# Kernel optimization log

Hardware: AMD Instinct MI355X
Metric: run time of the kernel (lower is better)

The kernel has to match this reference:

```python
import jax, jax.numpy as jnp
import numpy as np

N = 50000
E = 800000
DIM = 256
HEADS = 4
HDIM = DIM // HEADS  # 64
NEG_SLOPE = 0.2
LN_EPS = 1e-5


def _layernorm(x, g, b):
    mu = jnp.mean(x, axis=-1, keepdims=True)
    var = jnp.var(x, axis=-1, keepdims=True)
    return (x - mu) * jax.lax.rsqrt(var + LN_EPS) * g + b


def setup_inputs() -> dict:
    key = jax.random.key(0)
    ks = jax.random.split(key, 10)
    x = jax.random.normal(ks[0], (N, DIM), dtype=jnp.float32)
    edge_index = jax.random.randint(ks[1], (2, E), 0, N, dtype=jnp.int64)
    s = 0.05
    W = jax.random.normal(ks[2], (DIM, DIM), dtype=jnp.float32) * s       # GAT linear (heads*out = dim)
    a_src = jax.random.normal(ks[3], (HEADS, HDIM), dtype=jnp.float32) * s
    a_dst = jax.random.normal(ks[4], (HEADS, HDIM), dtype=jnp.float32) * s
    gat_b = jnp.zeros((DIM,), dtype=jnp.float32)
    ln_g = jnp.ones((DIM,), dtype=jnp.float32)
    ln_b = jnp.zeros((DIM,), dtype=jnp.float32)
    W1 = jax.random.normal(ks[5], (DIM, 4 * DIM), dtype=jnp.float32) * s
    b1 = jnp.zeros((4 * DIM,), dtype=jnp.float32)
    W2 = jax.random.normal(ks[6], (4 * DIM, DIM), dtype=jnp.float32) * s
    b2 = jnp.zeros((DIM,), dtype=jnp.float32)
    return {"x": x, "edge_index": edge_index, "W": W, "a_src": a_src,
            "a_dst": a_dst, "gat_b": gat_b, "ln_g": ln_g, "ln_b": ln_b,
            "W1": W1, "b1": b1, "W2": W2, "b2": b2}


def _gat(x, edge_index, W, a_src, a_dst, gat_b):
    # project and split heads: [N, H, C]
    h = (x @ W).reshape(N, HEADS, HDIM)
    alpha_src = jnp.einsum('nhc,hc->nh', h, a_src)  # [N, H]
    alpha_dst = jnp.einsum('nhc,hc->nh', h, a_dst)  # [N, H]
    src = edge_index[0]
    dst = edge_index[1]
    e = jax.nn.leaky_relu(alpha_src[src] + alpha_dst[dst], NEG_SLOPE)  # [E, H]
    # segment softmax over edges sharing a destination node
    m = jax.ops.segment_max(e, dst, num_segments=N)                   # [N, H]
    ex = jnp.exp(e - m[dst])
    denom = jax.ops.segment_sum(ex, dst, num_segments=N)              # [N, H]
    alpha = ex / (denom[dst] + 1e-16)                                 # [E, H]
    msg = h[src] * alpha[:, :, None]                                  # [E, H, C]
    out = jax.ops.segment_sum(msg.reshape(E, DIM), dst, num_segments=N)
    return out + gat_b


def reference(x, edge_index, W, a_src, a_dst, gat_b, ln_g, ln_b, W1, b1, W2, b2):
    residual = x
    g = _gat(x, edge_index, W, a_src, a_dst, gat_b)
    x = _layernorm(x + g, ln_g, ln_b)
    ffn = jax.nn.gelu(x @ W1 + b1, approximate=False) @ W2 + b2
    x = _layernorm(x + ffn, ln_g, ln_b)  # same norm params reused, as in source
    return x + residual
```

## Files before the change

### kernel.cpp

```cpp
#include <hip/hip_runtime.h>
#include <hip/hip_bf16.h>
#include <math.h>

typedef __bf16 bf16;
typedef bf16 bf16x8 __attribute__((ext_vector_type(8)));
typedef float floatx4 __attribute__((ext_vector_type(4)));

#define NN 50000
#define EE 800000
#define DIMC 256
#define FFC 1024

typedef __attribute__((address_space(3))) unsigned int lds_u32;
typedef __attribute__((address_space(1))) unsigned int gbl_u32;

static __device__ __forceinline__ void glds16(const bf16* g, bf16* l) {
    __builtin_amdgcn_global_load_lds((const gbl_u32*)g, (lds_u32*)l, 16, 0, 0);
}

static __device__ __forceinline__ unsigned short f2b(float f) {
    bf16 b = (bf16)f;
    return __builtin_bit_cast(unsigned short, b);
}
static __device__ __forceinline__ float b2f_lo(unsigned u) { return __uint_as_float(u << 16); }
static __device__ __forceinline__ float b2f_hi(unsigned u) { return __uint_as_float(u & 0xffff0000u); }

static __device__ __forceinline__ float gelu_f(float v) {
    float z = -1.5957691216f * v - 0.0713548163f * v * v * v;
    return v / (1.f + __expf(z));
}

__global__ __launch_bounds__(256)
void k_cast_bf16(const float* __restrict__ in, bf16* __restrict__ out, long n4) {
    long i = (long)blockIdx.x * 256 + threadIdx.x;
    if (i >= n4) return;
    float4 v = ((const float4*)in)[i];
    uint2 p;
    p.x = (unsigned)f2b(v.x) | ((unsigned)f2b(v.y) << 16);
    p.y = (unsigned)f2b(v.z) | ((unsigned)f2b(v.w) << 16);
    ((uint2*)out)[i] = p;
}

__global__ __launch_bounds__(256)
void k_tcast(const float* __restrict__ in, bf16* __restrict__ out, int K, int Nc) {
    __shared__ float t[32][33];
    int n0 = blockIdx.x * 32, k0 = blockIdx.y * 32;
    int tx = threadIdx.x & 31, ty = threadIdx.x >> 5;
#pragma unroll
    for (int i = 0; i < 4; ++i)
        t[ty + i * 8][tx] = in[(long)(k0 + ty + i * 8) * Nc + n0 + tx];
    __syncthreads();
#pragma unroll
    for (int i = 0; i < 4; ++i)
        out[(long)(n0 + ty + i * 8) * K + k0 + tx] = (bf16)t[tx][ty + i * 8];
}

template <int EPI>
__global__ __launch_bounds__(256)
void k_gemmA(const bf16* __restrict__ A, const bf16* __restrict__ BT,
             bf16* __restrict__ C, const float* __restrict__ bias,
             const float* __restrict__ avs, const float* __restrict__ avd,
             float* __restrict__ asrcO, float* __restrict__ adstO,
             int M, int K, int Nc) {
    __shared__ __attribute__((aligned(16))) bf16 smem[17408];
    bf16* As = smem;
    bf16* Bs = smem + 8192;
    const int tid = threadIdx.x;
    const int w = tid >> 6, lane = tid & 63;
    const int gm = blockIdx.x * 128, gn = blockIdx.y * 128;
    const int wm = (w >> 1) * 64, wn = (w & 1) * 64;
    const int lr = lane & 15, lkc = lane >> 4;

    long aoff[4], boff[4];
#pragma unroll
    for (int j = 0; j < 4; ++j) {
        int s = w * 4 + j;
        int r = s * 8 + (lane >> 3);
        int kc = ((lane & 7) ^ (r & 7)) * 8;
        aoff[j] = (long)min(gm + r, M - 1) * K + kc;
        boff[j] = (long)(gn + r) * K + kc;
    }

    floatx4 acc[4][4];
#pragma unroll
    for (int a = 0; a < 4; ++a)
#pragma unroll
        for (int b = 0; b < 4; ++b) acc[a][b] = floatx4{0.f, 0.f, 0.f, 0.f};

    for (int k0 = 0; k0 < K; k0 += 64) {
        if (k0) __syncthreads();
#pragma unroll
        for (int j = 0; j < 4; ++j) {
            int s = w * 4 + j;
            glds16(A + aoff[j] + k0, As + s * 512);
            glds16(BT + boff[j] + k0, Bs + s * 512);
        }
        __syncthreads();
#pragma unroll
        for (int kk = 0; kk < 2; ++kk) {
            bf16x8 af[4], bv[4];
#pragma unroll
            for (int mi = 0; mi < 4; ++mi) {
                int r = wm + mi * 16 + lr;
                int ch = (kk * 4 + lkc) ^ (r & 7);
                af[mi] = *(const bf16x8*)(As + r * 64 + ch * 8);
            }
#pragma unroll
            for (int ni = 0; ni < 4; ++ni) {
                int r = wn + ni * 16 + lr;
                int ch = (kk * 4 + lkc) ^ (r & 7);
                bv[ni] = *(const bf16x8*)(Bs + r * 64 + ch * 8);
            }
#pragma unroll
            for (int mi = 0; mi < 4; ++mi)
#pragma unroll
                for (int ni = 0; ni < 4; ++ni)
                    acc[mi][ni] = __builtin_amdgcn_mfma_f32_16x16x32_bf16(af[mi], bv[ni], acc[mi][ni], 0, 0, 0);
        }
    }

    __syncthreads();
    bf16* cs = smem;
#pragma unroll
    for (int ni = 0; ni < 4; ++ni) {
        const int cl = wn + ni * 16 + lr;
        const float bvs = (EPI == 1) ? bias[gn + cl] : 0.f;
#pragma unroll
        for (int mi = 0; mi < 4; ++mi)
#pragma unroll
            for (int i = 0; i < 4; ++i) {
                int rl = wm + mi * 16 + lkc * 4 + i;
                float v = acc[mi][ni][i] + bvs;
                if (EPI == 1) v = gelu_f(v);
                cs[rl * 136 + cl] = (bf16)v;
            }
    }
    __syncthreads();

    const int c8 = (lane & 15) * 8;
    float as8[8], ad8[8];
    int hd = 0;
    if (EPI == 0) {
        hd = (gn >> 6) + ((lane & 15) >> 3);
        const int cb = hd * 64 + (c8 & 63);
#pragma unroll
        for (int i = 0; i < 8; ++i) { as8[i] = avs[cb + i]; ad8[i] = avd[cb + i]; }
    }

#pragma unroll
    for (int t = 0; t < 8; ++t) {
        int rl = w * 32 + t * 4 + (lane >> 4);
        int grow = gm + rl;
        uint4 val = *(const uint4*)(cs + rl * 136 + c8);
        if (grow < M) *(uint4*)(C + (long)grow * Nc + gn + c8) = val;
        if (EPI == 0) {
            float h0 = b2f_lo(val.x), h1 = b2f_hi(val.x), h2 = b2f_lo(val.y), h3 = b2f_hi(val.y);
            float h4 = b2f_lo(val.z), h5 = b2f_hi(val.z), h6 = b2f_lo(val.w), h7 = b2f_hi(val.w);
            float ds = h0 * as8[0] + h1 * as8[1] + h2 * as8[2] + h3 * as8[3]
                     + h4 * as8[4] + h5 * as8[5] + h6 * as8[6] + h7 * as8[7];
            float dd = h0 * ad8[0] + h1 * ad8[1] + h2 * ad8[2] + h3 * ad8[3]
                     + h4 * ad8[4] + h5 * ad8[5] + h6 * ad8[6] + h7 * ad8[7];
#pragma unroll
            for (int off = 1; off < 8; off <<= 1) { ds += __shfl_xor(ds, off); dd += __shfl_xor(dd, off); }
            if ((lane & 7) == 0 && grow < M) {
                asrcO[grow * 4 + hd] = ds;
                adstO[grow * 4 + hd] = dd;
            }
        }
    }
}

__global__ __launch_bounds__(256)
void k_ffn2(const bf16* __restrict__ act, const bf16* __restrict__ W2T,
            const float* __restrict__ b2, const bf16* __restrict__ x1b,
            const float* __restrict__ x, const float* __restrict__ lng,
            const float* __restrict__ lnb, float* __restrict__ out, int M) {
    __shared__ __attribute__((aligned(16))) bf16 smem[20480];
    bf16* As2 = smem;
    bf16* Bs2 = smem + 4096;
    const int tid = threadIdx.x;
    const int w = tid >> 6, lane = tid & 63;
    const int gm = blockIdx.x * 64;
    const int wc = w * 64;
    const int lr = lane & 15, quad = lane >> 4;

    long goff[10];
#pragma unroll
    for (int j = 0; j < 10; ++j) {
        int s = w * 10 + j;
        int r7 = lane >> 3;
        if (s < 8) {
            int r = s * 8 + r7;
            int gc = ((lane & 7) ^ (r & 7)) * 8;
            goff[j] = (long)min(gm + r, M - 1) * FFC + gc;
        } else {
            int rb = (s - 8) * 8 + r7;
            int gc = ((lane & 7) ^ (rb & 7)) * 8;
            goff[j] = (long)rb * FFC + gc;
        }
    }

    floatx4 acc[4][4];
#pragma unroll
    for (int a = 0; a < 4; ++a)
#pragma unroll
        for (int b = 0; b < 4; ++b) acc[a][b] = floatx4{0.f, 0.f, 0.f, 0.f};

    for (int k0 = 0; k0 < FFC; k0 += 64) {
        if (k0) __syncthreads();
#pragma unroll
        for (int j = 0; j < 10; ++j) {
            int s = w * 10 + j;
            if (s < 8) glds16(act + goff[j] + k0, As2 + s * 512);
            else       glds16(W2T + goff[j] + k0, Bs2 + (s - 8) * 512);
        }
        __syncthreads();
#pragma unroll
        for (int kk = 0; kk < 2; ++kk) {
            bf16x8 af[4], bv[4];
#pragma unroll
            for (int mi = 0; mi < 4; ++mi) {
                int r = mi * 16 + lr;
                int ch = (kk * 4 + quad) ^ (r & 7);
                af[mi] = *(const bf16x8*)(As2 + r * 64 + ch * 8);
            }
#pragma unroll
            for (int ni = 0; ni < 4; ++ni) {
                int rb = wc + ni * 16 + lr;
                int ch = (kk * 4 + quad) ^ (rb & 7);
                bv[ni] = *(const bf16x8*)(Bs2 + rb * 64 + ch * 8);
            }
#pragma unroll
            for (int mi = 0; mi < 4; ++mi)
#pragma unroll
                for (int ni = 0; ni < 4; ++ni)
                    acc[mi][ni] = __builtin_amdgcn_mfma_f32_16x16x32_bf16(af[mi], bv[ni], acc[mi][ni], 0, 0, 0);
        }
    }

    __syncthreads();
    bf16* cs = smem;
#pragma unroll
    for (int ni = 0; ni < 4; ++ni) {
        const int col = wc + ni * 16 + lr;
        const float bvs = b2[col];
#pragma unroll
        for (int mi = 0; mi < 4; ++mi)
#pragma unroll
            for (int i = 0; i < 4; ++i) {
                int rl = mi * 16 + quad * 4 + i;
                cs[rl * 264 + col] = (bf16)(acc[mi][ni][i] + bvs);
            }
    }
    __syncthreads();
    float4 g4 = *(const float4*)(lng + lane * 4);
    float4 lb4 = *(const float4*)(lnb + lane * 4);
#pragma unroll 1
    for (int t = 0; t < 16; ++t) {
        int r = w * 16 + t;
        int grow = gm + r;
        long base = (long)min(grow, M - 1) * DIMC + lane * 4;
        uint2 cu = *(const uint2*)(cs + r * 264 + lane * 4);
        uint2 xu = *(const uint2*)(x1b + base);
        float v0 = b2f_lo(cu.x) + b2f_lo(xu.x);
        float v1 = b2f_hi(cu.x) + b2f_hi(xu.x);
        float v2 = b2f_lo(cu.y) + b2f_lo(xu.y);
        float v3 = b2f_hi(cu.y) + b2f_hi(xu.y);
        float s1 = v0 + v1 + v2 + v3;
        float s2 = v0 * v0 + v1 * v1 + v2 * v2 + v3 * v3;
#pragma unroll
        for (int off = 1; off < 64; off <<= 1) { s1 += __shfl_xor(s1, off); s2 += __shfl_xor(s2, off); }
        float mu = s1 * (1.f / DIMC);
        float rs = rsqrtf(s2 * (1.f / DIMC) - mu * mu + 1e-5f);
        float4 xr = *(const float4*)(x + base);
        float4 o;
        o.x = (v0 - mu) * rs * g4.x + lb4.x + xr.x;
        o.y = (v1 - mu) * rs * g4.y + lb4.y + xr.y;
        o.z = (v2 - mu) * rs * g4.z + lb4.z + xr.z;
        o.w = (v3 - mu) * rs * g4.w + lb4.w + xr.w;
        if (grow < M) *(float4*)(out + (long)grow * DIMC + lane * 4) = o;
    }
}

__global__ __launch_bounds__(256)
void k_count(const int* __restrict__ dst, unsigned* __restrict__ deg) {
    int e = blockIdx.x * 256 + threadIdx.x;
    if (e < EE) atomicAdd(&deg[dst[e]], 1u);
}

__global__ __launch_bounds__(1024)
void k_scan(const unsigned* __restrict__ deg, unsigned* __restrict__ rowoff,
            unsigned* __restrict__ cursor) {
    __shared__ unsigned wsum[16], wscan[16];
    __shared__ unsigned carry;
    int tid = threadIdx.x, lane = tid & 63, wid = tid >> 6;
    if (tid == 0) carry = 0;
    __syncthreads();
    for (int base = 0; base < NN; base += 1024) {
        int i = base + tid;
        unsigned v = (i < NN) ? deg[i] : 0u;
        unsigned s = v;
        for (int off = 1; off < 64; off <<= 1) {
            unsigned t = __shfl_up(s, off);
            if (lane >= off) s += t;
        }
        if (lane == 63) wsum[wid] = s;
        __syncthreads();
        if (wid == 0) {
            unsigned t = (lane < 16) ? wsum[lane] : 0u;
            unsigned ts = t;
            for (int off = 1; off < 16; off <<= 1) {
                unsigned u2 = __shfl_up(ts, off);
                if (lane >= off) ts += u2;
            }
            if (lane < 16) wscan[lane] = ts;
        }
        __syncthreads();
        unsigned basew = (wid > 0) ? wscan[wid - 1] : 0u;
        unsigned excl = carry + basew + (s - v);
        if (i < NN) { rowoff[i] = excl; cursor[i] = excl; }
        __syncthreads();
        if (tid == 0) carry += wscan[15];
        __syncthreads();
    }
    if (tid == 0) rowoff[NN] = carry;
}

__global__ __launch_bounds__(256)
void k_fill(const int* __restrict__ src, const int* __restrict__ dst,
            unsigned* __restrict__ cursor, unsigned* __restrict__ elist) {
    int e = blockIdx.x * 256 + threadIdx.x;
    if (e < EE) {
        unsigned p = atomicAdd(&cursor[dst[e]], 1u);
        elist[p] = (unsigned)src[e];
    }
}

__global__ __launch_bounds__(256)
void k_agg_ln1(const unsigned* __restrict__ rowoff, const unsigned* __restrict__ elist,
               const float* __restrict__ asrc, const float* __restrict__ adst,
               const bf16* __restrict__ hb, const float* __restrict__ x,
               const float* __restrict__ gatb, const float* __restrict__ lng,
               const float* __restrict__ lnb, bf16* __restrict__ x1b) {
    int node = (blockIdx.x * 256 + threadIdx.x) >> 6;
    int lane = threadIdx.x & 63;
    if (node >= NN) return;
    int beg = (int)rowoff[node], end = (int)rowoff[node + 1];
    int head = lane >> 4;
    float ad = adst[node * 4 + head];
    const int c = lane * 4;
    const bf16* hc = hb + c;
    const int bl = lane & 48;

    float dsum = 0.f;
    float a0 = 0.f, a1 = 0.f, a2 = 0.f, a3 = 0.f;

    for (int c0 = beg; c0 < end; c0 += 16) {
        int take = end - c0; if (take > 16) take = 16;
        int jj = c0 + (lane & 15);
        float ex = 0.f; int s = 0;
        if (jj < end) {
            s = (int)elist[jj];
            float e = asrc[s * 4 + head] + ad;
            e = (e > 0.f) ? e : 0.2f * e;
            ex = __expf(e);
        }
        dsum += ex;
        if (take == 16) {
#pragma unroll
            for (int j = 0; j < 16; ++j) {
                float al = __shfl(ex, bl + j);
                int sj = __shfl(s, bl + j);
                uint2 u = *(const uint2*)(hc + (long)sj * DIMC);
                a0 += al * b2f_lo(u.x);
                a1 += al * b2f_hi(u.x);
                a2 += al * b2f_lo(u.y);
                a3 += al * b2f_hi(u.y);
            }
        } else {
            for (int j = 0; j < take; ++j) {
                float al = __shfl(ex, bl + j);
                int sj = __shfl(s, bl + j);
                uint2 u = *(const uint2*)(hc + (long)sj * DIMC);
                a0 += al * b2f_lo(u.x);
                a1 += al * b2f_hi(u.x);
                a2 += al * b2f_lo(u.y);
                a3 += al * b2f_hi(u.y);
            }
        }
    }
    dsum += __shfl_xor(dsum, 1);
    dsum += __shfl_xor(dsum, 2);
    dsum += __shfl_xor(dsum, 4);
    dsum += __shfl_xor(dsum, 8);
    float invd = 1.f / (dsum + 1e-16f);
    a0 *= invd; a1 *= invd; a2 *= invd; a3 *= invd;

    long base = (long)node * DIMC + c;
    float4 xr = *(const float4*)(x + base);
    float4 gb = *(const float4*)(gatb + c);
    float v0 = xr.x + a0 + gb.x;
    float v1 = xr.y + a1 + gb.y;
    float v2 = xr.z + a2 + gb.z;
    float v3 = xr.w + a3 + gb.w;
    float s1 = v0 + v1 + v2 + v3;
    float s2 = v0 * v0 + v1 * v1 + v2 * v2 + v3 * v3;
    for (int off = 1; off < 64; off <<= 1) { s1 += __shfl_xor(s1, off); s2 += __shfl_xor(s2, off); }
    float mu = s1 * (1.f / DIMC);
    float rs = rsqrtf(s2 * (1.f / DIMC) - mu * mu + 1e-5f);
    float4 g4 = *(const float4*)(lng + c);
    float4 b4 = *(const float4*)(lnb + c);
    float y0 = (v0 - mu) * rs * g4.x + b4.x;
    float y1 = (v1 - mu) * rs * g4.y + b4.y;
    float y2 = (v2 - mu) * rs * g4.z + b4.z;
    float y3 = (v3 - mu) * rs * g4.w + b4.w;
    uint2 p;
    p.x = (unsigned)f2b(y0) | ((unsigned)f2b(y1) << 16);
    p.y = (unsigned)f2b(y2) | ((unsigned)f2b(y3) << 16);
    *(uint2*)(x1b + base) = p;
}

extern "C" void kernel_launch(void* const* d_in, const int* in_sizes, int n_in,
                              void* d_out, int out_size, void* d_ws, size_t ws_size,
                              hipStream_t stream) {
    const float* x    = (const float*)d_in[0];
    const int*   ei   = (const int*)d_in[1];
    const float* W    = (const float*)d_in[2];
    const float* a_s  = (const float*)d_in[3];
    const float* a_d  = (const float*)d_in[4];
    const float* gatb = (const float*)d_in[5];
    const float* lng  = (const float*)d_in[6];
    const float* lnb  = (const float*)d_in[7];
    const float* W1   = (const float*)d_in[8];
    const float* b1   = (const float*)d_in[9];
    const float* W2   = (const float*)d_in[10];
    const float* b2   = (const float*)d_in[11];
    float* out = (float*)d_out;
    char* ws = (char*)d_ws;

    bf16*     xb     = (bf16*)(ws + 0L);
    bf16*     hb     = (bf16*)(ws + 25600000L);
    bf16*     x1b    = (bf16*)(ws + 51200000L);
    bf16*     act    = (bf16*)(ws + 76800000L);
    float*    asrc   = (float*)(ws + 179200000L);
    float*    adst   = (float*)(ws + 180000000L);
    unsigned* deg    = (unsigned*)(ws + 180800000L);
    unsigned* cursor = (unsigned*)(ws + 181000192L);
    unsigned* rowoff = (unsigned*)(ws + 181200384L);
    unsigned* elist  = (unsigned*)(ws + 181400832L);
    bf16*     WT     = (bf16*)(ws + 184600832L);
    bf16*     W1T    = (bf16*)(ws + 184731904L);
    bf16*     W2T    = (bf16*)(ws + 185256192L);

    const int* esrc = ei;
    const int* edst = ei + EE;

    hipMemsetAsync(deg, 0, NN * sizeof(unsigned), stream);
    k_cast_bf16<<<12500, 256, 0, stream>>>(x, xb, (long)NN * DIMC / 4);
    {
        dim3 gw(DIMC / 32, DIMC / 32);
        k_tcast<<<gw, 256, 0, stream>>>(W, WT, DIMC, DIMC);
        dim3 gw1(FFC / 32, DIMC / 32);
        k_tcast<<<gw1, 256, 0, stream>>>(W1, W1T, DIMC, FFC);
        dim3 gw2(DIMC / 32, FFC / 32);
        k_tcast<<<gw2, 256, 0, stream>>>(W2, W2T, FFC, DIMC);
    }

    dim3 g1(391, 2);
    k_gemmA<0><<<g1, 256, 0, stream>>>(xb, WT, hb, nullptr, a_s, a_d, asrc, adst, NN, DIMC, DIMC);

    k_count<<<3125, 256, 0, stream>>>(edst, deg);
    k_scan<<<1, 1024, 0, stream>>>(deg, rowoff, cursor);
    k_fill<<<3125, 256, 0, stream>>>(esrc, edst, cursor, elist);

    k_agg_ln1<<<12500, 256, 0, stream>>>(rowoff, elist, asrc, adst, hb, x, gatb, lng, lnb, x1b);

    dim3 g2(391, 8);
    k_gemmA<1><<<g2, 256, 0, stream>>>(x1b, W1T, act, b1, nullptr, nullptr, nullptr, nullptr, NN, DIMC, FFC);

    k_ffn2<<<782, 256, 0, stream>>>(act, W2T, b2, x1b, x, lng, lnb, out, NN);
}
```

Before: 503.6 us.

## Fuse FFN up-projection, GELU and down-projection into one kernel

```diff
diff --git a/kernel.cpp b/kernel.cpp
--- a/kernel.cpp
+++ b/kernel.cpp
@@ -170,94 +170,102 @@
     }
 }
 
-__global__ __launch_bounds__(256)
-void k_ffn2(const bf16* __restrict__ act, const bf16* __restrict__ W2T,
-            const float* __restrict__ b2, const bf16* __restrict__ x1b,
-            const float* __restrict__ x, const float* __restrict__ lng,
-            const float* __restrict__ lnb, float* __restrict__ out, int M) {
-    __shared__ __attribute__((aligned(16))) bf16 smem[20480];
-    bf16* As2 = smem;
-    bf16* Bs2 = smem + 4096;
+__global__ __launch_bounds__(512)
+void k_ffn(const bf16* __restrict__ x1b, const bf16* __restrict__ W1T,
+           const bf16* __restrict__ W2T, const float* __restrict__ b1,
+           const float* __restrict__ b2, const float* __restrict__ x,
+           const float* __restrict__ lng, const float* __restrict__ lnb,
+           float* __restrict__ out, int M) {
+    __shared__ __attribute__((aligned(16))) bf16 smem[18432];
+    bf16* acts = smem;
+    bf16* w1s  = smem + 2048;
+    bf16* w2s  = smem + 10240;
     const int tid = threadIdx.x;
     const int w = tid >> 6, lane = tid & 63;
+    const int lr = lane & 15, lkc = lane >> 4;
+    const int mg = w >> 1, nh = w & 1;
     const int gm = blockIdx.x * 64;
-    const int wc = w * 64;
-    const int lr = lane & 15, quad = lane >> 4;
-
-    long goff[10];
-#pragma unroll
-    for (int j = 0; j < 10; ++j) {
-        int s = w * 10 + j;
-        int r7 = lane >> 3;
-        if (s < 8) {
-            int r = s * 8 + r7;
-            int gc = ((lane & 7) ^ (r & 7)) * 8;
-            goff[j] = (long)min(gm + r, M - 1) * FFC + gc;
-        } else {
-            int rb = (s - 8) * 8 + r7;
-            int gc = ((lane & 7) ^ (rb & 7)) * 8;
-            goff[j] = (long)rb * FFC + gc;
-        }
-    }
-
-    floatx4 acc[4][4];
-#pragma unroll
-    for (int a = 0; a < 4; ++a)
-#pragma unroll
-        for (int b = 0; b < 4; ++b) acc[a][b] = floatx4{0.f, 0.f, 0.f, 0.f};
-
-    for (int k0 = 0; k0 < FFC; k0 += 64) {
-        if (k0) __syncthreads();
-#pragma unroll
-        for (int j = 0; j < 10; ++j) {
-            int s = w * 10 + j;
-            if (s < 8) glds16(act + goff[j] + k0, As2 + s * 512);
-            else       glds16(W2T + goff[j] + k0, Bs2 + (s - 8) * 512);
-        }
-        __syncthreads();
-#pragma unroll
-        for (int kk = 0; kk < 2; ++kk) {
-            bf16x8 af[4], bv[4];
-#pragma unroll
-            for (int mi = 0; mi < 4; ++mi) {
-                int r = mi * 16 + lr;
-                int ch = (kk * 4 + quad) ^ (r & 7);
-                af[mi] = *(const bf16x8*)(As2 + r * 64 + ch * 8);
-            }
-#pragma unroll
-            for (int ni = 0; ni < 4; ++ni) {
-                int rb = wc + ni * 16 + lr;
-                int ch = (kk * 4 + quad) ^ (rb & 7);
-                bv[ni] = *(const bf16x8*)(Bs2 + rb * 64 + ch * 8);
-            }
-#pragma unroll
-            for (int mi = 0; mi < 4; ++mi)
-#pragma unroll
-                for (int ni = 0; ni < 4; ++ni)
-                    acc[mi][ni] = __builtin_amdgcn_mfma_f32_16x16x32_bf16(af[mi], bv[ni], acc[mi][ni], 0, 0, 0);
+
+    bf16x8 xf[8];
+    {
+        long rb = (long)min(gm + mg * 16 + lr, M - 1) * DIMC;
+#pragma unroll
+        for (int kf = 0; kf < 8; ++kf)
+            xf[kf] = *(const bf16x8*)(x1b + rb + kf * 32 + lkc * 8);
+    }
+
+    floatx4 accB[8];
+#pragma unroll
+    for (int i = 0; i < 8; ++i) accB[i] = floatx4{0.f, 0.f, 0.f, 0.f};
+
+    for (int c = 0; c < 32; ++c) {
+        if (c) __syncthreads();
+#pragma unroll
+        for (int j = 0; j < 2; ++j) {
+            int sg = w * 2 + j;
+            int r = sg * 2 + (lane >> 5);
+            int col = ((lane & 31) ^ (r & 7)) * 8;
+            glds16(W1T + (long)(c * 32 + r) * DIMC + col, w1s + sg * 512);
+        }
+#pragma unroll
+        for (int j = 0; j < 2; ++j) {
+            int sg = w * 2 + j;
+            int r = sg * 16 + (lane >> 2);
+            int col = c * 32 + (((lane & 3) ^ ((r >> 1) & 3)) * 8);
+            glds16(W2T + (long)r * FFC + col, w2s + sg * 512);
+        }
+        __syncthreads();
+
+        floatx4 accA = floatx4{0.f, 0.f, 0.f, 0.f};
+        const int rbA = nh * 16 + lr;
+#pragma unroll
+        for (int kf = 0; kf < 8; ++kf) {
+            int g = (kf * 4 + lkc) ^ (rbA & 7);
+            bf16x8 bv = *(const bf16x8*)(w1s + rbA * 256 + g * 8);
+            accA = __builtin_amdgcn_mfma_f32_16x16x32_bf16(xf[kf], bv, accA, 0, 0, 0);
+        }
+        float b1v = b1[c * 32 + nh * 16 + lr];
+#pragma unroll
+        for (int i = 0; i < 4; ++i) {
+            int row = mg * 16 + lkc * 4 + i;
+            int colc = nh * 16 + lr;
+            int g = (colc >> 3) ^ ((row >> 1) & 3);
+            acts[row * 32 + g * 8 + (colc & 7)] = (bf16)gelu_f(accA[i] + b1v);
+        }
+        __syncthreads();
+
+        {
+            int ra = mg * 16 + lr;
+            int ga = lkc ^ ((ra >> 1) & 3);
+            bf16x8 af = *(const bf16x8*)(acts + ra * 32 + ga * 8);
+#pragma unroll
+            for (int ni = 0; ni < 8; ++ni) {
+                int rb = nh * 128 + ni * 16 + lr;
+                int gb = lkc ^ ((rb >> 1) & 3);
+                bf16x8 bv = *(const bf16x8*)(w2s + rb * 32 + gb * 8);
+                accB[ni] = __builtin_amdgcn_mfma_f32_16x16x32_bf16(af, bv, accB[ni], 0, 0, 0);
+            }
         }
     }
 
     __syncthreads();
     bf16* cs = smem;
 #pragma unroll
-    for (int ni = 0; ni < 4; ++ni) {
-        const int col = wc + ni * 16 + lr;
-        const float bvs = b2[col];
-#pragma unroll
-        for (int mi = 0; mi < 4; ++mi)
-#pragma unroll
-            for (int i = 0; i < 4; ++i) {
-                int rl = mi * 16 + quad * 4 + i;
-                cs[rl * 264 + col] = (bf16)(acc[mi][ni][i] + bvs);
-            }
+    for (int ni = 0; ni < 8; ++ni) {
+        int col = nh * 128 + ni * 16 + lr;
+        float b2v = b2[col];
+#pragma unroll
+        for (int i = 0; i < 4; ++i) {
+            int rl = mg * 16 + lkc * 4 + i;
+            cs[rl * 264 + col] = (bf16)(accB[ni][i] + b2v);
+        }
     }
     __syncthreads();
     float4 g4 = *(const float4*)(lng + lane * 4);
     float4 lb4 = *(const float4*)(lnb + lane * 4);
 #pragma unroll 1
-    for (int t = 0; t < 16; ++t) {
-        int r = w * 16 + t;
+    for (int t = 0; t < 8; ++t) {
+        int r = w * 8 + t;
         int grow = gm + r;
         long base = (long)min(grow, M - 1) * DIMC + lane * 4;
         uint2 cu = *(const uint2*)(cs + r * 264 + lane * 4);
@@ -441,7 +449,6 @@
     bf16*     xb     = (bf16*)(ws + 0L);
     bf16*     hb     = (bf16*)(ws + 25600000L);
     bf16*     x1b    = (bf16*)(ws + 51200000L);
-    bf16*     act    = (bf16*)(ws + 76800000L);
     float*    asrc   = (float*)(ws + 179200000L);
     float*    adst   = (float*)(ws + 180000000L);
     unsigned* deg    = (unsigned*)(ws + 180800000L);
@@ -475,8 +482,5 @@
 
     k_agg_ln1<<<12500, 256, 0, stream>>>(rowoff, elist, asrc, adst, hb, x, gatb, lng, lnb, x1b);
 
-    dim3 g2(391, 8);
-    k_gemmA<1><<<g2, 256, 0, stream>>>(x1b, W1T, act, b1, nullptr, nullptr, nullptr, nullptr, NN, DIMC, FFC);
-
-    k_ffn2<<<782, 256, 0, stream>>>(act, W2T, b2, x1b, x, lng, lnb, out, NN);
-}
+    k_ffn<<<782, 512, 0, stream>>>(x1b, W1T, W2T, b1, b2, x, lng, lnb, out, NN);
+}
```

Result: no change. 502.0 us (-0.3%).
